# Performance work log

Measured on AMD Instinct MI355X. Metric: run time of the kernel, lower is better.

Reference implementation:

```python
import jax, jax.numpy as jnp
import numpy as np

N = 100000        # nodes
E = 1600000       # edges (avg degree 16)
F = 128           # num_features
H = 8             # heads
D = F // H        # head_dim


def setup_inputs() -> dict:
    key = jax.random.key(0)
    ks = jax.random.split(key, 11)
    s = 1.0 / np.sqrt(F)
    return {
        "feat": jax.random.normal(ks[0], (N, F), dtype=jnp.float32),
        "edge_src": jax.random.randint(ks[1], (E,), 0, N, dtype=jnp.int32),
        "edge_dst": jax.random.randint(ks[2], (E,), 0, N, dtype=jnp.int32),
        "Wq": jax.random.uniform(ks[3], (F, F), jnp.float32, -s, s),
        "bq": jax.random.uniform(ks[4], (F,), jnp.float32, -s, s),
        "Wk": jax.random.uniform(ks[5], (F, F), jnp.float32, -s, s),
        "bk": jax.random.uniform(ks[6], (F,), jnp.float32, -s, s),
        "Wv": jax.random.uniform(ks[7], (F, F), jnp.float32, -s, s),
        "bv": jax.random.uniform(ks[8], (F,), jnp.float32, -s, s),
        "Wo": jax.random.uniform(ks[9], (F, F), jnp.float32, -s, s),
        "bo": jax.random.uniform(ks[10], (F,), jnp.float32, -s, s),
    }


def reference(feat, edge_src, edge_dst, Wq, bq, Wk, bk, Wv, bv, Wo, bo):
    scale = D ** -0.5
    # projections, split into heads: [N, H, D]
    q = ((feat @ Wq.T + bq) * scale).reshape(N, H, D)
    k = (feat @ Wk.T + bk).reshape(N, H, D)
    v = (feat @ Wv.T + bv).reshape(N, H, D)

    # per-edge dot product k[src] . q[dst] -> [E, H]  (dfn.u_dot_v)
    scores = jnp.einsum('ehd,ehd->eh', k[edge_src], q[edge_dst])

    # edge softmax normalized over incoming edges of each dst node
    m = jax.ops.segment_max(scores, edge_dst, num_segments=N)  # [N, H]
    m = jnp.where(jnp.isfinite(m), m, 0.0)
    e = jnp.exp(scores - m[edge_dst])                          # [E, H]
    z = jax.ops.segment_sum(e, edge_dst, num_segments=N)       # [N, H]
    alpha = e / z[edge_dst]                                    # [E, H]

    # weighted sum aggregation (u_mul_e + sum): [N, H, D]
    wv = alpha[:, :, None] * v[edge_src]                       # [E, H, D]
    attn = jax.ops.segment_sum(wv, edge_dst, num_segments=N)

    return attn.reshape(N, F) @ Wo.T + bo
```

## Files before the change

### kernel.cpp

```cpp
#include <hip/hip_runtime.h>
#include <math.h>

#define N_NODES 100000
#define N_EDGES 1600000
#define FDIM 128
#define NHEAD 8
#define HDIM 16
#define SCAT_PHASES 4
#define CNT_STRIDE 16

using bf16x8 = __attribute__((ext_vector_type(8))) short;
using half8  = __attribute__((ext_vector_type(8))) _Float16;
using f32x4  = __attribute__((ext_vector_type(4))) float;
using f32x2  = __attribute__((ext_vector_type(2))) float;

__device__ inline unsigned short f2bf(float f) {
    union { float f; unsigned int u; } x; x.f = f;
    unsigned int u = x.u;
    return (unsigned short)((u + 0x7fffu + ((u >> 16) & 1u)) >> 16);
}
__device__ inline unsigned short f2h(float f) {
    _Float16 h = (_Float16)f;
    return __builtin_bit_cast(unsigned short, h);
}
__device__ inline unsigned int packh2(float a, float b) {
    return (unsigned int)f2h(a) | ((unsigned int)f2h(b) << 16);
}
__device__ inline float h_lo(unsigned int u) {
    return (float)__builtin_bit_cast(_Float16, (unsigned short)(u & 0xffffu));
}
__device__ inline float h_hi(unsigned int u) {
    return (float)__builtin_bit_cast(_Float16, (unsigned short)(u >> 16));
}
__device__ inline float exp2_fast(float x) {
#if __has_builtin(__builtin_amdgcn_exp2f)
    return __builtin_amdgcn_exp2f(x);
#else
    return __expf(x * 0.6931471805599453f);
#endif
}

#if __has_builtin(__builtin_amdgcn_cvt_pk_fp8_f32)
__device__ inline unsigned char fp8_enc(float x) {
    return (unsigned char)(__builtin_amdgcn_cvt_pk_fp8_f32(x, x, 0, false) & 0xff);
}
#else
__device__ inline unsigned char fp8_enc(float x) {
    unsigned int u = __builtin_bit_cast(unsigned int, x);
    unsigned int s = (u >> 24) & 0x80;
    float ax = fabsf(x);
    if (!(ax >= 0.001953125f)) {
        int m = (int)(ax * 512.f + 0.5f);
        return (unsigned char)(s | (unsigned)(m > 7 ? 7 : m));
    }
    if (ax > 448.f) return (unsigned char)(s | 0x7e);
    int e; float fr = frexpf(ax, &e);
    int q = (int)(fr * 16.f + 0.5f);
    if (q == 16) { q = 8; e += 1; }
    int exp = e - 1 + 7;
    if (exp <= 0) { int m = (int)(ax * 512.f + 0.5f); return (unsigned char)(s | (unsigned)(m > 7 ? 7 : m)); }
    if (exp > 15) return (unsigned char)(s | 0x7e);
    return (unsigned char)(s | (exp << 3) | (q & 7));
}
#endif

#if __has_builtin(__builtin_amdgcn_cvt_pk_f32_fp8)
#define FP8_HW_DECODE 1
#else
__device__ inline float fp8_dec_sw(unsigned char b) {
    int s = b >> 7, e = (b >> 3) & 15, m = b & 7;
    float v = (e == 0) ? ldexpf((float)m, -9) : ldexpf((float)(8 + m), e - 10);
    return s ? -v : v;
}
#endif

__device__ inline float dot_fp8_16(uint4 kr, const f32x2* __restrict__ qq2) {
#ifdef FP8_HW_DECODE
    f32x2 a = {0.f, 0.f};
    f32x2 p;
    p = __builtin_amdgcn_cvt_pk_f32_fp8(kr.x, false); a += p * qq2[0];
    p = __builtin_amdgcn_cvt_pk_f32_fp8(kr.x, true);  a += p * qq2[1];
    p = __builtin_amdgcn_cvt_pk_f32_fp8(kr.y, false); a += p * qq2[2];
    p = __builtin_amdgcn_cvt_pk_f32_fp8(kr.y, true);  a += p * qq2[3];
    p = __builtin_amdgcn_cvt_pk_f32_fp8(kr.z, false); a += p * qq2[4];
    p = __builtin_amdgcn_cvt_pk_f32_fp8(kr.z, true);  a += p * qq2[5];
    p = __builtin_amdgcn_cvt_pk_f32_fp8(kr.w, false); a += p * qq2[6];
    p = __builtin_amdgcn_cvt_pk_f32_fp8(kr.w, true);  a += p * qq2[7];
    return a[0] + a[1];
#else
    const float* qq = (const float*)qq2;
    float s = 0.f;
    unsigned int wds[4] = {kr.x, kr.y, kr.z, kr.w};
#pragma unroll
    for (int i = 0; i < 4; ++i)
#pragma unroll
        for (int j = 0; j < 4; ++j)
            s = fmaf(fp8_dec_sw((wds[i] >> (8 * j)) & 0xff), qq[i * 4 + j], s);
    return s;
#endif
}

__global__ __launch_bounds__(256) void convert_w_kernel(
    const float* __restrict__ W0, const float* __restrict__ W1,
    const float* __restrict__ W2, const float* __restrict__ W3,
    unsigned short* __restrict__ out, int* __restrict__ cnt)
{
    int i = blockIdx.x * 256 + threadIdx.x;
    int j  = i & 7;
    int l  = (i >> 3) & 63;
    int fk = i >> 9;
    int ks = fk & 3, nf = fk >> 2;
    int s = (nf * 16 + (l & 15)) * FDIM + ks * 32 + (l >> 4) * 8 + j;
    out[i]             = f2bf(W0[s]);
    out[16384 + i]     = f2bf(W1[s]);
    out[2 * 16384 + i] = f2bf(W2[s]);
    out[3 * 16384 + i] = f2h(W3[s]);
    for (int c = i; c < N_NODES; c += 64 * 256)
        cnt[(size_t)c * CNT_STRIDE] = 0;
}

__global__ void count_rank_kernel(const int* __restrict__ dst, int* __restrict__ cnt,
                                  unsigned int* __restrict__ pk, int n)
{
    int i = blockIdx.x * 256 + threadIdx.x;
    if (i < n) {
        int d = __builtin_nontemporal_load(&dst[i]);
        unsigned r = (unsigned)atomicAdd(&cnt[(size_t)d * CNT_STRIDE], 1);
        pk[i] = ((unsigned)d << 8) | (r & 0xffu);
    }
}

struct GemmArgs {
    const unsigned short* W[3];
    const float* b[3];
    void* out[3];
    float scale[3];
};

template<int NP, bool IN_F32, bool MFMA_F16, int OUTM>
__global__ __launch_bounds__(256, 2) void mfma_gemm_v2(
    const void* __restrict__ Ain, GemmArgs ga, int nrows)
{
    __shared__ unsigned short A_s[128][136];
    __shared__ unsigned short W_sh[8192];

    const int t  = threadIdx.x;
    const int r0 = blockIdx.x * 128;

#pragma unroll
    for (int it = 0; it < 8; ++it) {
        int i = t + it * 256;
        int r = i >> 4, c8 = (i & 15) << 3;
        int gr = r0 + r;
        if (IN_F32) {
            float4 v0 = make_float4(0.f, 0.f, 0.f, 0.f), v1 = v0;
            if (gr < nrows) {
                const float* Af = (const float*)Ain;
                v0 = *(const float4*)&Af[(size_t)gr * FDIM + c8];
                v1 = *(const float4*)&Af[(size_t)gr * FDIM + c8 + 4];
            }
            uint4 pk;
            pk.x = (unsigned)f2bf(v0.x) | ((unsigned)f2bf(v0.y) << 16);
            pk.y = (unsigned)f2bf(v0.z) | ((unsigned)f2bf(v0.w) << 16);
            pk.z = (unsigned)f2bf(v1.x) | ((unsigned)f2bf(v1.y) << 16);
            pk.w = (unsigned)f2bf(v1.z) | ((unsigned)f2bf(v1.w) << 16);
            *(uint4*)&A_s[r][c8] = pk;
        } else {
            uint4 v = make_uint4(0u, 0u, 0u, 0u);
            if (gr < nrows) {
                const unsigned short* Ab = (const unsigned short*)Ain;
                v = *(const uint4*)&Ab[(size_t)gr * FDIM + c8];
            }
            *(uint4*)&A_s[r][c8] = v;
        }
    }
    __syncthreads();

    const int w  = t >> 6, l = t & 63;
    const int lr = l & 15, lk = l >> 4;

    bf16x8 a[2][4];
#pragma unroll
    for (int rg = 0; rg < 2; ++rg)
#pragma unroll
        for (int ks = 0; ks < 4; ++ks)
            a[rg][ks] = *(const bf16x8*)&A_s[w * 32 + rg * 16 + lr][ks * 32 + lk * 8];

#pragma unroll
    for (int p = 0; p < NP; ++p) {
        const unsigned short* Wsrc = ga.W[p];
        f32x4 acc[2][8];
#pragma unroll
        for (int rg = 0; rg < 2; ++rg)
#pragma unroll
            for (int nf = 0; nf < 8; ++nf) acc[rg][nf] = (f32x4){0.f, 0.f, 0.f, 0.f};

#pragma unroll
        for (int h = 0; h < 2; ++h) {
#pragma unroll
            for (int it = 0; it < 4; ++it) {
                int chunk = t + it * 256;
                *(uint4*)&W_sh[chunk * 8] = *(const uint4*)&Wsrc[h * 8192 + chunk * 8];
            }
            __syncthreads();
#pragma unroll
            for (int nfl = 0; nfl < 4; ++nfl) {
                int nf = h * 4 + nfl;
#pragma unroll
                for (int ks = 0; ks < 4; ++ks) {
                    bf16x8 bfr = *(const bf16x8*)&W_sh[((nfl * 4 + ks) * 64 + l) * 8];
                    if (MFMA_F16) {
                        acc[0][nf] = __builtin_amdgcn_mfma_f32_16x16x32_f16(
                            __builtin_bit_cast(half8, a[0][ks]), __builtin_bit_cast(half8, bfr),
                            acc[0][nf], 0, 0, 0);
                        acc[1][nf] = __builtin_amdgcn_mfma_f32_16x16x32_f16(
                            __builtin_bit_cast(half8, a[1][ks]), __builtin_bit_cast(half8, bfr),
                            acc[1][nf], 0, 0, 0);
                    } else {
                        acc[0][nf] = __builtin_amdgcn_mfma_f32_16x16x32_bf16(a[0][ks], bfr, acc[0][nf], 0, 0, 0);
                        acc[1][nf] = __builtin_amdgcn_mfma_f32_16x16x32_bf16(a[1][ks], bfr, acc[1][nf], 0, 0, 0);
                    }
                }
            }
            __syncthreads();
        }

        const float* bias = ga.b[p];
        const float  scl  = ga.scale[p];
        const int    mode = (OUTM >> (2 * p)) & 3;

        if (mode == 0) {
            unsigned short* Oh = &A_s[0][0];
#pragma unroll
            for (int rg = 0; rg < 2; ++rg)
#pragma unroll
                for (int nf = 0; nf < 8; ++nf) {
                    int col = nf * 16 + lr;
                    float bv = bias[col];
#pragma unroll
                    for (int j = 0; j < 4; ++j)
                        Oh[(w * 32 + rg * 16 + lk * 4 + j) * 136 + col] = f2h((acc[rg][nf][j] + bv) * scl);
                }
            __syncthreads();
            unsigned short* outp = (unsigned short*)ga.out[p];
#pragma unroll
            for (int it = 0; it < 8; ++it) {
                int i = t + it * 256;
                int r = i >> 4, c8 = (i & 15) << 3;
                if (r0 + r < nrows)
                    *(uint4*)&outp[(size_t)(r0 + r) * FDIM + c8] = *(const uint4*)&Oh[r * 136 + c8];
            }
        } else if (mode == 1) {
            unsigned char* O8 = (unsigned char*)A_s;
#pragma unroll
            for (int rg = 0; rg < 2; ++rg)
#pragma unroll
                for (int nf = 0; nf < 8; ++nf) {
                    int col = nf * 16 + lr;
                    float bv = bias[col];
#pragma unroll
                    for (int j = 0; j < 4; ++j)
                        O8[(w * 32 + rg * 16 + lk * 4 + j) * 144 + col] = fp8_enc((acc[rg][nf][j] + bv) * scl);
                }
            __syncthreads();
            unsigned char* outp = (unsigned char*)ga.out[p];
#pragma unroll
            for (int it = 0; it < 4; ++it) {
                int i = t + it * 256;
                int r = i >> 3, c16 = (i & 7) << 4;
                if (r0 + r < nrows)
                    *(uint4*)&outp[(size_t)(r0 + r) * FDIM + c16] = *(const uint4*)&O8[r * 144 + c16];
            }
        } else {
            float* outp = (float*)ga.out[p];
#pragma unroll
            for (int rg = 0; rg < 2; ++rg)
#pragma unroll
                for (int nf = 0; nf < 8; ++nf) {
                    int col = nf * 16 + lr;
                    float bv = bias[col];
                    int row = r0 + w * 32 + rg * 16 + lk * 4;
#pragma unroll
                    for (int j = 0; j < 4; ++j)
                        if (row + j < nrows)
                            outp[(size_t)(row + j) * FDIM + col] = (acc[rg][nf][j] + bv) * scl;
                }
        }
    }
}

__global__ void scan_a_kernel(const int* __restrict__ cnt, int* __restrict__ row_off,
                              int* __restrict__ part, int n)
{
    __shared__ int s[256];
    int t = threadIdx.x;
    int gid = blockIdx.x * 256 + t;
    int x = (gid < n) ? cnt[(size_t)gid * CNT_STRIDE] : 0;
    s[t] = x;
    __syncthreads();
    for (int off = 1; off < 256; off <<= 1) {
        int val = (t >= off) ? s[t - off] : 0;
        __syncthreads();
        s[t] += val;
        __syncthreads();
    }
    if (gid < n) row_off[gid] = s[t] - x;
    if (t == 255) part[blockIdx.x] = s[255];
}

__global__ void scan_b_kernel(int* __restrict__ part, int nb)
{
    __shared__ int s[512];
    int t = threadIdx.x;
    int x = (t < nb) ? part[t] : 0;
    s[t] = x;
    __syncthreads();
    for (int off = 1; off < 512; off <<= 1) {
        int val = (t >= off) ? s[t - off] : 0;
        __syncthreads();
        s[t] += val;
        __syncthreads();
    }
    if (t < nb) part[t] = s[t] - x;
}

__global__ void scatter_all_kernel(const int* __restrict__ src,
                                   const unsigned int* __restrict__ pk,
                                   const int* __restrict__ row_off,
                                   const int* __restrict__ part,
                                   int* __restrict__ csr_src, int n, int blocksPerPhase)
{
    int phase = blockIdx.x / blocksPerPhase;
    int i = (blockIdx.x % blocksPerPhase) * 256 + threadIdx.x;
    if (i >= n) return;
    int lo = (int)((long long)N_NODES * phase / SCAT_PHASES);
    int hi = (int)((long long)N_NODES * (phase + 1) / SCAT_PHASES);
    unsigned p = __builtin_nontemporal_load(&pk[i]);
    int d = (int)(p >> 8);
    if (d >= lo && d < hi) {
        int pos = row_off[d] + part[d >> 8] + (int)(p & 0xffu);
        csr_src[pos] = __builtin_nontemporal_load(&src[i]);
    }
}

__global__ __launch_bounds__(256) void attn_kernel(
    const unsigned short* __restrict__ q, const unsigned char* __restrict__ kf8,
    const unsigned short* __restrict__ v,
    const int* __restrict__ row_off, const int* __restrict__ part,
    const int* __restrict__ csr_src,
    unsigned short* __restrict__ out, int nnodes, int nedges)
{
    __shared__ float q_s[4][NHEAD][18];
    __shared__ float p_s[4][64][NHEAD];
    __shared__ int   src_s[4][64];

    const int w = threadIdx.x >> 6;
    const int l = threadIdx.x & 63;
    const int node = blockIdx.x * 4 + w;
    if (node >= nnodes) return;

    {
        unsigned int qv = *(const unsigned int*)&q[(size_t)node * FDIM + l * 2];
        *(f32x2*)&q_s[w][l >> 3][(l & 7) * 2] = (f32x2){h_lo(qv), h_hi(qv)};
    }

    const int e_l = l >> 3, h_sc = l & 7;
    const int e2 = l >> 4, h_ag = (l >> 1) & 7, dq = l & 1;
    const int vo = h_ag * HDIM + dq * 8;

    const int start = row_off[node] + part[node >> 8];
    const int end   = (node == nnodes - 1) ? nedges
                      : row_off[node + 1] + part[(node + 1) >> 8];

    float z_run = 0.f;
    f32x2 acc[4] = {{0.f,0.f},{0.f,0.f},{0.f,0.f},{0.f,0.f}};

    const f32x2* qq2 = (const f32x2*)&q_s[w][h_sc][0];

    for (int c0 = start; c0 < end; c0 += 64) {
        const int cn = min(64, end - c0);

        for (int i = l; i < cn; i += 64)
            src_s[w][i] = csr_src[c0 + i];

        for (int base = 0; base < cn; base += 32) {
            uint4 kr[4];
#pragma unroll
            for (int it = 0; it < 4; ++it) {
                int ei = base + it * 8 + e_l;
                if (ei < cn)
                    kr[it] = *(const uint4*)&kf8[(size_t)src_s[w][ei] * FDIM + h_sc * 16];
            }
#pragma unroll
            for (int it = 0; it < 4; ++it) {
                int ei = base + it * 8 + e_l;
                if (ei < cn) {
                    float p = exp2_fast(dot_fp8_16(kr[it], qq2));
                    p_s[w][ei][h_sc] = p;
                    z_run += p;
                }
            }
        }

        for (int base = 0; base < cn; base += 4) {
            int e  = base + e2;
            int ec = min(e, cn - 1);
            float p = (e < cn) ? p_s[w][e][h_ag] : 0.f;
            uint4 vv = *(const uint4*)&v[(size_t)src_s[w][ec] * FDIM + vo];
            f32x2 p2 = {p, p};
            acc[0] += p2 * (f32x2){h_lo(vv.x), h_hi(vv.x)};
            acc[1] += p2 * (f32x2){h_lo(vv.y), h_hi(vv.y)};
            acc[2] += p2 * (f32x2){h_lo(vv.z), h_hi(vv.z)};
            acc[3] += p2 * (f32x2){h_lo(vv.w), h_hi(vv.w)};
        }
    }

#pragma unroll
    for (int mask = 8; mask < 64; mask <<= 1)
        z_run += __shfl_xor(z_run, mask, 64);

#pragma unroll
    for (int mask = 16; mask < 64; mask <<= 1)
#pragma unroll
        for (int i = 0; i < 4; ++i) {
            acc[i][0] += __shfl_xor(acc[i][0], mask, 64);
            acc[i][1] += __shfl_xor(acc[i][1], mask, 64);
        }

    float z_ag = __shfl(z_run, h_ag, 64);

    if (e2 == 0) {
        uint4 o = make_uint4(0u, 0u, 0u, 0u);
        if (end > start) {
            float rz = 1.0f / z_ag;
            o.x = packh2(acc[0][0] * rz, acc[0][1] * rz);
            o.y = packh2(acc[1][0] * rz, acc[1][1] * rz);
            o.z = packh2(acc[2][0] * rz, acc[2][1] * rz);
            o.w = packh2(acc[3][0] * rz, acc[3][1] * rz);
        }
        *(uint4*)&out[(size_t)node * FDIM + vo] = o;
    }
}

extern "C" void kernel_launch(void* const* d_in, const int* in_sizes, int n_in,
                              void* d_out, int out_size, void* d_ws, size_t ws_size,
                              hipStream_t stream)
{
    const float* feat = (const float*)d_in[0];
    const int*   esrc = (const int*)d_in[1];
    const int*   edst = (const int*)d_in[2];
    const float* Wq   = (const float*)d_in[3];
    const float* bq   = (const float*)d_in[4];
    const float* Wk   = (const float*)d_in[5];
    const float* bk   = (const float*)d_in[6];
    const float* Wv   = (const float*)d_in[7];
    const float* bv   = (const float*)d_in[8];
    const float* Wo   = (const float*)d_in[9];
    const float* bo   = (const float*)d_in[10];
    float* out = (float*)d_out;

    const size_t NROW = (size_t)N_NODES * FDIM;
    unsigned short* qb  = (unsigned short*)d_ws;
    unsigned short* vb  = qb + NROW;
    unsigned short* ab  = vb + NROW;
    unsigned char*  kf8 = (unsigned char*)(ab + NROW);
    unsigned short* wbf = (unsigned short*)(kf8 + NROW);
    unsigned int* pk = (unsigned int*)(wbf + 4 * 16384);
    int* cnt     = (int*)(pk + N_EDGES);
    int* row_off = cnt + (size_t)N_NODES * CNT_STRIDE;
    int* part    = row_off + N_NODES + 1;
    int* csr_src = part + 512;

    const int gemmGrid = (N_NODES + 127) / 128;
    const int edgeGrid = (N_EDGES + 255) / 256;
    const int nb       = (N_NODES + 255) / 256;

    hipLaunchKernelGGL(convert_w_kernel, dim3(64), dim3(256), 0, stream,
                       Wq, Wk, Wv, Wo, wbf, cnt);

    hipLaunchKernelGGL(count_rank_kernel, dim3(edgeGrid), dim3(256), 0, stream,
                       edst, cnt, pk, N_EDGES);

    GemmArgs qkv;
    qkv.W[0] = wbf;          qkv.b[0] = bq; qkv.out[0] = qb;  qkv.scale[0] = 0.25f * 1.4426950408889634f;
    qkv.W[1] = wbf + 16384;  qkv.b[1] = bk; qkv.out[1] = kf8; qkv.scale[1] = 1.0f;
    qkv.W[2] = wbf + 32768;  qkv.b[2] = bv; qkv.out[2] = vb;  qkv.scale[2] = 1.0f;
    hipLaunchKernelGGL((mfma_gemm_v2<3, true, false, 4>), dim3(gemmGrid), dim3(256), 0, stream,
                       feat, qkv, N_NODES);

    hipLaunchKernelGGL(scan_a_kernel, dim3(nb), dim3(256), 0, stream, cnt, row_off, part, N_NODES);
    hipLaunchKernelGGL(scan_b_kernel, dim3(1), dim3(512), 0, stream, part, nb);

    hipLaunchKernelGGL(scatter_all_kernel, dim3(edgeGrid * SCAT_PHASES), dim3(256), 0, stream,
                       esrc, pk, row_off, part, csr_src, N_EDGES, edgeGrid);

    hipLaunchKernelGGL(attn_kernel, dim3((N_NODES + 3) / 4), dim3(256), 0, stream,
                       qb, kf8, vb, row_off, part, csr_src, ab, N_NODES, N_EDGES);

    GemmArgs oprj;
    oprj.W[0] = wbf + 3 * 16384; oprj.b[0] = bo; oprj.out[0] = out; oprj.scale[0] = 1.0f;
    hipLaunchKernelGGL((mfma_gemm_v2<1, false, true, 2>), dim3(gemmGrid), dim3(256), 0, stream,
                       ab, oprj, N_NODES);
}
```

Before: 272.1 us.

## Partition edge rank counting by XCD with per-XCD work tickets and byte ranks

Replaces the per-edge global-atomic count/rank kernel with a persistent kernel. Each workgroup reads its XCC_ID and claims 4096-edge chunks from a per-XCD ticket counter. Every XCD scans all edges but only counts destinations in its own node slice, so the counter atomics stay in one XCD's L2 and can use workgroup scope instead of going through cross-die coherence. Ranks are stored as one byte per edge, and the scatter kernel re-reads dst directly instead of a packed 32-bit word. The trade-off is that edge_dst is read eight times. Correctness also depends on the hardware XCC_ID mapping and on workgroup-scope atomics being coherent within an XCD.

Result: slower. 285.0 us (+4.8%).

```diff
diff --git a/kernel.cpp b/kernel.cpp
--- a/kernel.cpp
+++ b/kernel.cpp
@@ -8,6 +8,9 @@
 #define HDIM 16
 #define SCAT_PHASES 4
 #define CNT_STRIDE 16
+#define NXCD 8
+#define NODES_PER_XCD (N_NODES / NXCD)
+#define CHUNK_EDGES 4096
 
 using bf16x8 = __attribute__((ext_vector_type(8))) short;
 using half8  = __attribute__((ext_vector_type(8))) _Float16;
@@ -103,7 +106,7 @@
 __global__ __launch_bounds__(256) void convert_w_kernel(
     const float* __restrict__ W0, const float* __restrict__ W1,
     const float* __restrict__ W2, const float* __restrict__ W3,
-    unsigned short* __restrict__ out, int* __restrict__ cnt)
+    unsigned short* __restrict__ out, int* __restrict__ cnt, int* __restrict__ tick)
 {
     int i = blockIdx.x * 256 + threadIdx.x;
     int j  = i & 7;
@@ -117,16 +120,57 @@
     out[3 * 16384 + i] = f2h(W3[s]);
     for (int c = i; c < N_NODES; c += 64 * 256)
         cnt[(size_t)c * CNT_STRIDE] = 0;
-}
-
-__global__ void count_rank_kernel(const int* __restrict__ dst, int* __restrict__ cnt,
-                                  unsigned int* __restrict__ pk, int n)
-{
-    int i = blockIdx.x * 256 + threadIdx.x;
-    if (i < n) {
-        int d = __builtin_nontemporal_load(&dst[i]);
-        unsigned r = (unsigned)atomicAdd(&cnt[(size_t)d * CNT_STRIDE], 1);
-        pk[i] = ((unsigned)d << 8) | (r & 0xffu);
+    if (i < NXCD * CNT_STRIDE) tick[i] = 0;
+}
+
+__global__ __launch_bounds__(256) void count_rank_xcd_kernel(
+    const int* __restrict__ edst, int* __restrict__ cnt,
+    unsigned char* __restrict__ rank8, int* __restrict__ tick, int n)
+{
+    __shared__ int c_s;
+    unsigned xcd;
+    asm("s_getreg_b32 %0, hwreg(HW_REG_XCC_ID, 0, 4)" : "=s"(xcd));
+    xcd &= (NXCD - 1);
+    const int lo = (int)xcd * NODES_PER_XCD;
+    const int hi = lo + NODES_PER_XCD;
+
+    for (;;) {
+        if (threadIdx.x == 0)
+            c_s = __hip_atomic_fetch_add(&tick[xcd * CNT_STRIDE], 1,
+                                         __ATOMIC_RELAXED, __HIP_MEMORY_SCOPE_WORKGROUP);
+        __syncthreads();
+        const int base = c_s * CHUNK_EDGES;
+        __syncthreads();
+        if (base >= n) break;
+
+#pragma unroll
+        for (int g = 0; g < 4; ++g) {
+            int i0 = base + threadIdx.x * 4 + g * 1024;
+            if (i0 + 3 < n) {
+                int4 d4 = *(const int4*)&edst[i0];
+#pragma unroll
+                for (int u = 0; u < 4; ++u) {
+                    int d = (&d4.x)[u];
+                    if (d >= lo && d < hi) {
+                        int r = __hip_atomic_fetch_add(&cnt[(size_t)d * CNT_STRIDE], 1,
+                                                       __ATOMIC_RELAXED, __HIP_MEMORY_SCOPE_WORKGROUP);
+                        rank8[i0 + u] = (unsigned char)r;
+                    }
+                }
+            } else {
+                for (int u = 0; u < 4; ++u) {
+                    int idx = i0 + u;
+                    if (idx < n) {
+                        int d = edst[idx];
+                        if (d >= lo && d < hi) {
+                            int r = __hip_atomic_fetch_add(&cnt[(size_t)d * CNT_STRIDE], 1,
+                                                           __ATOMIC_RELAXED, __HIP_MEMORY_SCOPE_WORKGROUP);
+                            rank8[idx] = (unsigned char)r;
+                        }
+                    }
+                }
+            }
+        }
     }
 }
 
@@ -324,8 +368,8 @@
     if (t < nb) part[t] = s[t] - x;
 }
 
-__global__ void scatter_all_kernel(const int* __restrict__ src,
-                                   const unsigned int* __restrict__ pk,
+__global__ void scatter_all_kernel(const int* __restrict__ src, const int* __restrict__ dst,
+                                   const unsigned char* __restrict__ rank8,
                                    const int* __restrict__ row_off,
                                    const int* __restrict__ part,
                                    int* __restrict__ csr_src, int n, int blocksPerPhase)
@@ -333,12 +377,11 @@
     int phase = blockIdx.x / blocksPerPhase;
     int i = (blockIdx.x % blocksPerPhase) * 256 + threadIdx.x;
     if (i >= n) return;
-    int lo = (int)((long long)N_NODES * phase / SCAT_PHASES);
-    int hi = (int)((long long)N_NODES * (phase + 1) / SCAT_PHASES);
-    unsigned p = __builtin_nontemporal_load(&pk[i]);
-    int d = (int)(p >> 8);
+    int lo = (N_NODES / SCAT_PHASES) * phase;
+    int hi = lo + N_NODES / SCAT_PHASES;
+    int d = __builtin_nontemporal_load(&dst[i]);
     if (d >= lo && d < hi) {
-        int pos = row_off[d] + part[d >> 8] + (int)(p & 0xffu);
+        int pos = row_off[d] + part[d >> 8] + (int)__builtin_nontemporal_load(&rank8[i]);
         csr_src[pos] = __builtin_nontemporal_load(&src[i]);
     }
 }
@@ -465,9 +508,10 @@
     unsigned short* ab  = vb + NROW;
     unsigned char*  kf8 = (unsigned char*)(ab + NROW);
     unsigned short* wbf = (unsigned short*)(kf8 + NROW);
-    unsigned int* pk = (unsigned int*)(wbf + 4 * 16384);
-    int* cnt     = (int*)(pk + N_EDGES);
-    int* row_off = cnt + (size_t)N_NODES * CNT_STRIDE;
+    unsigned char* rank8 = (unsigned char*)(wbf + 4 * 16384);
+    int* cnt     = (int*)(rank8 + ((N_EDGES + 63) & ~63));
+    int* tick    = cnt + (size_t)N_NODES * CNT_STRIDE;
+    int* row_off = tick + NXCD * CNT_STRIDE;
     int* part    = row_off + N_NODES + 1;
     int* csr_src = part + 512;
 
@@ -476,10 +520,10 @@
     const int nb       = (N_NODES + 255) / 256;
 
     hipLaunchKernelGGL(convert_w_kernel, dim3(64), dim3(256), 0, stream,
-                       Wq, Wk, Wv, Wo, wbf, cnt);
-
-    hipLaunchKernelGGL(count_rank_kernel, dim3(edgeGrid), dim3(256), 0, stream,
-                       edst, cnt, pk, N_EDGES);
+                       Wq, Wk, Wv, Wo, wbf, cnt, tick);
+
+    hipLaunchKernelGGL(count_rank_xcd_kernel, dim3(2048), dim3(256), 0, stream,
+                       edst, cnt, rank8, tick, N_EDGES);
 
     GemmArgs qkv;
     qkv.W[0] = wbf;          qkv.b[0] = bq; qkv.out[0] = qb;  qkv.scale[0] = 0.25f * 1.4426950408889634f;
@@ -492,7 +536,7 @@
     hipLaunchKernelGGL(scan_b_kernel, dim3(1), dim3(512), 0, stream, part, nb);
 
     hipLaunchKernelGGL(scatter_all_kernel, dim3(edgeGrid * SCAT_PHASES), dim3(256), 0, stream,
-                       esrc, pk, row_off, part, csr_src, N_EDGES, edgeGrid);
+                       esrc, edst, rank8, row_off, part, csr_src, N_EDGES, edgeGrid);
 
     hipLaunchKernelGGL(attn_kernel, dim3((N_NODES + 3) / 4), dim3(256), 0, stream,
                        qb, kf8, vb, row_off, part, csr_src, ab, N_NODES, N_EDGES);
```
